# Performance work log

Hardware: AMD Instinct MI355X
Metric: run time of the kernel (lower is better)

Reference implementation:

```python
import jax, jax.numpy as jnp
import numpy as np

D_MODEL = 2048
N_HEADS = 16
D_K = D_MODEL // N_HEADS


def setup_inputs() -> dict:
    key = jax.random.key(0)
    ks = jax.random.split(key, 9)
    s = 1.0 / np.sqrt(D_MODEL)
    def lin(k):
        kw, kb = jax.random.split(k)
        W = jax.random.uniform(kw, (D_MODEL, D_MODEL), jnp.float32, -s, s)
        b = jax.random.uniform(kb, (D_MODEL,), jnp.float32, -s, s)
        return W, b
    Wq, bq = lin(ks[0])
    Wk, bk = lin(ks[1])
    Wv, bv = lin(ks[2])
    Wo, bo = lin(ks[3])
    x = jax.random.normal(ks[4], (2, 2048, D_MODEL), jnp.float32)
    return {"x": x, "Wq": Wq, "bq": bq, "Wk": Wk, "bk": bk,
            "Wv": Wv, "bv": bv, "Wo": Wo, "bo": bo}


def _mha(x, Wq, bq, Wk, bk, Wv, bv, Wo, bo):
    B, S, _ = x.shape
    # Linear projections (torch Linear: x @ W.T + b), split into heads: b s (h d) -> b h s d
    def proj(W, b):
        y = jnp.einsum('bsm,nm->bsn', x, W) + b
        return y.reshape(B, S, N_HEADS, D_K).transpose(0, 2, 1, 3)
    q = proj(Wq, bq)
    k = proj(Wk, bk)
    v = proj(Wv, bv)
    scores = jnp.einsum('bhsd,bhtd->bhst', q, k) / jnp.sqrt(jnp.float32(D_K))
    causal = jnp.triu(jnp.ones((S, S), bool), k=1)  # True above diagonal -> masked
    scores = jnp.where(causal[None, None], -jnp.inf, scores)
    attn = jax.nn.softmax(scores, axis=-1)  # dropout p=0 (eval)
    out = jnp.einsum('bhst,bhtd->bhsd', attn, v)
    out = out.transpose(0, 2, 1, 3).reshape(B, S, D_MODEL)
    return jnp.einsum('bsm,nm->bsn', out, Wo) + bo


def reference(x, Wq, bq, Wk, bk, Wv, bv, Wo, bo):
    return _mha(x, Wq, bq, Wk, bk, Wv, bv, Wo, bo)
```

## Files before the change

kernel.cpp:

```cpp
#include <hip/hip_runtime.h>

typedef unsigned short u16;
typedef __attribute__((ext_vector_type(8))) short bf16x8;
typedef __attribute__((ext_vector_type(4))) float f32x4;
typedef __attribute__((ext_vector_type(4))) unsigned short u16x4;

__device__ __forceinline__ u16 f2bf(float f) {
  union { float f; unsigned u; } v; v.f = f;
  return (u16)((v.u + 0x7FFFu + ((v.u >> 16) & 1u)) >> 16);
}

__device__ __forceinline__ void gload16(const u16* g, u16* l) {
  __builtin_amdgcn_global_load_lds((const __attribute__((address_space(1))) void*)g,
                                   (__attribute__((address_space(3))) void*)l, 16, 0, 0);
}

__global__ __launch_bounds__(256) void k_f2bf5(
    const float* __restrict__ i0, const float* __restrict__ i1, const float* __restrict__ i2,
    const float* __restrict__ i3, const float* __restrict__ i4,
    u16* o0, u16* o1, u16* o2, u16* o3, u16* o4, int n4x, int n4w) {
  const int seg = blockIdx.y;
  const float* in = (seg == 0) ? i0 : (seg == 1) ? i1 : (seg == 2) ? i2 : (seg == 3) ? i3 : i4;
  u16* out = (seg == 0) ? o0 : (seg == 1) ? o1 : (seg == 2) ? o2 : (seg == 3) ? o3 : o4;
  const int n4 = (seg == 0) ? n4x : n4w;
  int i = blockIdx.x * 256 + threadIdx.x;
  const int stride = gridDim.x * 256;
  for (; i < n4; i += stride) {
    const float4 v = ((const float4*)in)[i];
    u16x4 o;
    o.x = f2bf(v.x); o.y = f2bf(v.y); o.z = f2bf(v.z); o.w = f2bf(v.w);
    ((u16x4*)out)[i] = o;
  }
}

template <int OUT_F32>
__global__ __launch_bounds__(256, 4) void k_gemm12(
    const u16* __restrict__ A, const u16* __restrict__ Bt,
    const float* __restrict__ b0, const float* __restrict__ b1, const float* __restrict__ b2,
    u16* __restrict__ C0, u16* __restrict__ C1, u16* __restrict__ C2,
    float* __restrict__ Cf, int NBM)
{
  __shared__ alignas(16) u16 As[8192];
  __shared__ alignas(16) u16 Bs[8192];

  const int tid = threadIdx.x;
  const int lane = tid & 63, wid = tid >> 6;
  const int fr = lane & 15, fg = lane >> 4;
  const int wr = wid >> 1, wc = wid & 1;

  const int nblk = gridDim.x;
  const int q = nblk >> 3, r = nblk & 7;
  const int xcd = blockIdx.x & 7, lid = blockIdx.x >> 3;
  const int wgid = (xcd < r ? xcd * (q + 1) : r * (q + 1) + (xcd - r) * q) + lid;
  const int mb = wgid % NBM, nb = wgid / NBM;
  const long row0 = (long)mb * 128;
  const long col0 = (long)nb * 128;

  int sRow[4], sCol[4];
#pragma unroll
  for (int i = 0; i < 4; ++i) {
    const int g = (wid * 4 + i) * 64 + lane;
    sRow[i] = g >> 3;
    sCol[i] = ((g & 7) ^ (sRow[i] & 7)) << 3;
  }

  const int sw = fr & 7;
  const int aBase = (wr * 64 + fr) * 64;
  const int bBase = (wc * 64 + fr) * 64;
  const int pc0 = (fg ^ sw) << 3;
  const int pc1 = ((4 + fg) ^ sw) << 3;

  f32x4 acc[4][4] = {};

#pragma unroll 1
  for (int t = 0; t < 32; ++t) {
    if (t) __syncthreads();
    const long k0 = (long)t << 6;
#pragma unroll
    for (int i = 0; i < 4; ++i) {
      gload16(A  + (row0 + sRow[i]) * 2048L + k0 + sCol[i], &As[(wid * 4 + i) * 512]);
      gload16(Bt + (col0 + sRow[i]) * 2048L + k0 + sCol[i], &Bs[(wid * 4 + i) * 512]);
    }
    __syncthreads();

#pragma unroll
    for (int kc = 0; kc < 2; ++kc) {
      const int pc = kc ? pc1 : pc0;
      bf16x8 a[4], b[4];
#pragma unroll
      for (int i = 0; i < 4; ++i) {
        a[i] = *(const bf16x8*)&As[aBase + i * 1024 + pc];
        b[i] = *(const bf16x8*)&Bs[bBase + i * 1024 + pc];
      }
#pragma unroll
      for (int i = 0; i < 4; ++i)
#pragma unroll
        for (int j = 0; j < 4; ++j)
          acc[i][j] = __builtin_amdgcn_mfma_f32_16x16x32_bf16(a[i], b[j], acc[i][j], 0, 0, 0);
    }
  }

  const int seg = (int)(col0 >> 11);
  const long colL = col0 & 2047;
  const float* bp = (seg == 0) ? b0 : (seg == 1) ? b1 : b2;
  u16* Cb = (seg == 0) ? C0 : (seg == 1) ? C1 : C2;
#pragma unroll
  for (int j = 0; j < 4; ++j) {
    const long cN = colL + wc * 64 + j * 16 + fr;
    const float bv = bp[cN];
#pragma unroll
    for (int i = 0; i < 4; ++i) {
      const long rM = row0 + wr * 64 + i * 16 + fg * 4;
#pragma unroll
      for (int reg = 0; reg < 4; ++reg) {
        const float v = acc[i][j][reg] + bv;
        if (OUT_F32) Cf[(rM + reg) * 2048 + cN] = v;
        else         Cb[(rM + reg) * 2048 + cN] = f2bf(v);
      }
    }
  }
}

__global__ __launch_bounds__(256) void k_transpose_v(const u16* __restrict__ V,
                                                     u16* __restrict__ Vt) {
  __shared__ u16 t[64][68];
  const int bh = blockIdx.z;
  const long s0 = (long)blockIdx.x * 64;
  const long d0 = (long)blockIdx.y * 64;
  const int tid = threadIdx.x;
  const long rowbase = (long)(bh >> 4) * 2048;
  const int hcol = (bh & 15) * 128;
#pragma unroll
  for (int i = 0; i < 4; ++i) {
    const int v = tid + i * 256;
    const int r = v >> 4, c4 = (v & 15) << 2;
    const u16x4 val = *(const u16x4*)&V[(rowbase + s0 + r) * 2048 + hcol + d0 + c4];
    *(u16x4*)&t[r][c4] = val;
  }
  __syncthreads();
#pragma unroll
  for (int i = 0; i < 4; ++i) {
    const int v = tid + i * 256;
    const int dr = v >> 4, s4 = (v & 15) << 2;
    u16x4 o;
    o.x = t[s4 + 0][dr]; o.y = t[s4 + 1][dr]; o.z = t[s4 + 2][dr]; o.w = t[s4 + 3][dr];
    *(u16x4*)&Vt[((long)bh * 128 + d0 + dr) * 2048 + s0 + s4] = o;
  }
}

__global__ __launch_bounds__(512) void k_flash_attn(
    const u16* __restrict__ Q, const u16* __restrict__ K, const u16* __restrict__ Vt,
    u16* __restrict__ O)
{
  __shared__ alignas(16) u16 Kt[2][8192];
  __shared__ alignas(16) u16 Vtt[2][8192];
  __shared__ alignas(16) u16 Plds[8][16][72];

  const int tid = threadIdx.x;
  const int lane = tid & 63, wid = tid >> 6;
  const int fr = lane & 15, fg = lane >> 4;

  const int L = blockIdx.x;
  const int bh = (L & 7) * 4 + ((L >> 3) & 3);
  const int bx = L >> 5;

  const long rowbase = (long)(bh >> 4) * 2048;
  const int hcol = (bh & 15) * 128;
  const u16* Kg = K + rowbase * 2048 + hcol;
  const u16* Vg = Vt + (long)bh * 128 * 2048;
  const float scale2 = 0.08838834764831845f * 1.44269504089f;

  int kR[2], kC[2], vR[2], vC[2];
#pragma unroll
  for (int i = 0; i < 2; ++i) {
    const int chunk = (wid * 2 + i) * 64 + lane;
    kR[i] = chunk >> 4;
    kC[i] = ((chunk & 15) ^ (kR[i] & 7)) << 3;
    vR[i] = chunk >> 3;
    vC[i] = ((chunk & 7) ^ (vR[i] & 7)) << 3;
  }

  const int sw = fr & 7;
  int kbase[4], vbase[2];
#pragma unroll
  for (int c = 0; c < 4; ++c) kbase[c] = fr * 128 + (((c * 4 + fg) ^ sw) << 3);
#pragma unroll
  for (int kc = 0; kc < 2; ++kc) vbase[kc] = fr * 64 + (((kc * 4 + fg) ^ sw) << 3);

  for (int pass = 0; pass < 2; ++pass) {
    const int qblk = pass ? (15 - bx) : bx;
    const int n = 2 * (qblk + 1);
    const int q_lo = qblk * 128 + wid * 16;

    bf16x8 qf[4];
#pragma unroll
    for (int c = 0; c < 4; ++c)
      qf[c] = *(const bf16x8*)&Q[(rowbase + q_lo + fr) * 2048 + hcol + c * 32 + fg * 8];

    f32x4 oacc[8] = {};
    float m_run[4], l_run[4];
#pragma unroll
    for (int r = 0; r < 4; ++r) { m_run[r] = -1e30f; l_run[r] = 0.0f; }

#pragma unroll
    for (int i = 0; i < 2; ++i) {
      gload16(Kg + (long)kR[i] * 2048 + kC[i], &Kt[0][(wid * 2 + i) * 512]);
      gload16(Vg + (long)vR[i] * 2048 + vC[i], &Vtt[0][(wid * 2 + i) * 512]);
    }

    int cur = 0;
    for (int j = 0; j < n; ++j) {
      if (j + 1 < n) {
        const long kv = (long)(j + 1) * 64;
#pragma unroll
        for (int i = 0; i < 2; ++i) {
          gload16(Kg + (kv + kR[i]) * 2048 + kC[i], &Kt[cur ^ 1][(wid * 2 + i) * 512]);
          gload16(Vg + (long)vR[i] * 2048 + kv + vC[i], &Vtt[cur ^ 1][(wid * 2 + i) * 512]);
        }
        asm volatile("s_waitcnt vmcnt(4)" ::: "memory");
      } else {
        asm volatile("s_waitcnt vmcnt(0)" ::: "memory");
      }
      __builtin_amdgcn_s_barrier();
      __builtin_amdgcn_sched_barrier(0);

      const int kvlo = j * 64;
      const bool skip = (kvlo >= q_lo + 16);
      if (!skip) {
        const bool needmask = (kvlo + 63 > q_lo);

        f32x4 st[4] = {};
        const u16* kt = Kt[cur];
#pragma unroll
        for (int t = 0; t < 4; ++t)
#pragma unroll
          for (int c = 0; c < 4; ++c) {
            const bf16x8 kf = *(const bf16x8*)&kt[kbase[c] + t * 2048];
            st[t] = __builtin_amdgcn_mfma_f32_16x16x32_bf16(qf[c], kf, st[t], 0, 0, 0);
          }

        float pmax[4] = {-1e30f, -1e30f, -1e30f, -1e30f};
        if (needmask) {
#pragma unroll
          for (int t = 0; t < 4; ++t) {
            const int kg = kvlo + t * 16 + fr;
#pragma unroll
            for (int r = 0; r < 4; ++r) {
              const int qg = q_lo + fg * 4 + r;
              const float v = (kg <= qg) ? st[t][r] * scale2 : -1e30f;
              st[t][r] = v;
              pmax[r] = fmaxf(pmax[r], v);
            }
          }
        } else {
#pragma unroll
          for (int t = 0; t < 4; ++t)
#pragma unroll
            for (int r = 0; r < 4; ++r) {
              const float v = st[t][r] * scale2;
              st[t][r] = v;
              pmax[r] = fmaxf(pmax[r], v);
            }
        }
#pragma unroll
        for (int d = 1; d < 16; d <<= 1)
#pragma unroll
          for (int r = 0; r < 4; ++r) pmax[r] = fmaxf(pmax[r], __shfl_xor(pmax[r], d));

        const int ok = (pmax[0] <= m_run[0] + 8.f) & (pmax[1] <= m_run[1] + 8.f) &
                       (pmax[2] <= m_run[2] + 8.f) & (pmax[3] <= m_run[3] + 8.f);
        if (!__all(ok)) {
#pragma unroll
          for (int r = 0; r < 4; ++r) {
            const float nm = fmaxf(m_run[r], pmax[r]);
            const float al = exp2f(m_run[r] - nm);
            l_run[r] *= al;
            m_run[r] = nm;
#pragma unroll
            for (int dt = 0; dt < 8; ++dt) oacc[dt][r] *= al;
          }
        }

        float lsum[4] = {0.f, 0.f, 0.f, 0.f};
#pragma unroll
        for (int t = 0; t < 4; ++t)
#pragma unroll
          for (int r = 0; r < 4; ++r) {
            const float p = exp2f(st[t][r] - m_run[r]);
            st[t][r] = p;
            lsum[r] += p;
          }
#pragma unroll
        for (int d = 1; d < 16; d <<= 1)
#pragma unroll
          for (int r = 0; r < 4; ++r) lsum[r] += __shfl_xor(lsum[r], d);
#pragma unroll
        for (int r = 0; r < 4; ++r) l_run[r] += lsum[r];

#pragma unroll
        for (int t = 0; t < 4; ++t)
#pragma unroll
          for (int r = 0; r < 4; ++r)
            Plds[wid][fg * 4 + r][t * 16 + fr] = f2bf(st[t][r]);
        asm volatile("s_waitcnt lgkmcnt(0)" ::: "memory");
        __builtin_amdgcn_sched_barrier(0);

        const u16* vt = Vtt[cur];
#pragma unroll
        for (int kc = 0; kc < 2; ++kc) {
          const bf16x8 pf = *(const bf16x8*)&Plds[wid][fr][kc * 32 + fg * 8];
#pragma unroll
          for (int dt = 0; dt < 8; ++dt) {
            const bf16x8 vf = *(const bf16x8*)&vt[vbase[kc] + dt * 1024];
            oacc[dt] = __builtin_amdgcn_mfma_f32_16x16x32_bf16(pf, vf, oacc[dt], 0, 0, 0);
          }
        }
      }

      asm volatile("" ::: "memory");
      __builtin_amdgcn_s_barrier();
      cur ^= 1;
    }

    float inv[4];
#pragma unroll
    for (int r = 0; r < 4; ++r) inv[r] = 1.0f / l_run[r];
#pragma unroll
    for (int dt = 0; dt < 8; ++dt)
#pragma unroll
      for (int r = 0; r < 4; ++r)
        O[(rowbase + q_lo + fg * 4 + r) * 2048 + hcol + dt * 16 + fr] = f2bf(oacc[dt][r] * inv[r]);
  }
}

extern "C" void kernel_launch(void* const* d_in, const int* in_sizes, int n_in,
                              void* d_out, int out_size, void* d_ws, size_t ws_size,
                              hipStream_t stream) {
  const float* x  = (const float*)d_in[0];
  const float* Wq = (const float*)d_in[1];
  const float* bq = (const float*)d_in[2];
  const float* Wk = (const float*)d_in[3];
  const float* bk = (const float*)d_in[4];
  const float* Wv = (const float*)d_in[5];
  const float* bv = (const float*)d_in[6];
  const float* Wo = (const float*)d_in[7];
  const float* bo = (const float*)d_in[8];
  float* out = (float*)d_out;

  char* ws = (char*)d_ws;
  const size_t SZ_X = 16777216;
  const size_t SZ_W = 8388608;
  u16* xb  = (u16*)(ws);
  u16* wqb = (u16*)(ws + SZ_X);
  u16* wkb = (u16*)(ws + SZ_X + 1 * SZ_W);
  u16* wvb = (u16*)(ws + SZ_X + 2 * SZ_W);
  u16* wob = (u16*)(ws + SZ_X + 3 * SZ_W);
  u16* Qb  = (u16*)(ws + 1 * SZ_X + 4 * SZ_W);
  u16* Kb  = (u16*)(ws + 2 * SZ_X + 4 * SZ_W);
  u16* Vb  = (u16*)(ws + 3 * SZ_X + 4 * SZ_W);
  u16* Vtb = (u16*)(ws + 4 * SZ_X + 4 * SZ_W);
  u16* Ob  = Vb;

  k_f2bf5<<<dim3(1024, 5), 256, 0, stream>>>(x, Wq, Wk, Wv, Wo,
                                             xb, wqb, wkb, wvb, wob,
                                             8388608 / 4, 4194304 / 4);

  k_gemm12<0><<<1536, 256, 0, stream>>>(xb, wqb, bq, bk, bv, Qb, Kb, Vb, nullptr, 32);

  k_transpose_v<<<dim3(32, 2, 32), 256, 0, stream>>>(Vb, Vtb);

  k_flash_attn<<<256, 512, 0, stream>>>(Qb, Kb, Vtb, Ob);

  k_gemm12<1><<<512, 256, 0, stream>>>(Ob, wob, bo, bo, bo, nullptr, nullptr, nullptr, out, 32);
}
```

Before: 280.1 us.

## Fuse V transpose into QKV GEMM epilogue and retile flash attention

```diff
diff --git a/kernel.cpp b/kernel.cpp
--- a/kernel.cpp
+++ b/kernel.cpp
@@ -37,7 +37,7 @@
 __global__ __launch_bounds__(256, 4) void k_gemm12(
     const u16* __restrict__ A, const u16* __restrict__ Bt,
     const float* __restrict__ b0, const float* __restrict__ b1, const float* __restrict__ b2,
-    u16* __restrict__ C0, u16* __restrict__ C1, u16* __restrict__ C2,
+    u16* __restrict__ C0, u16* __restrict__ C1, u16* __restrict__ Vt,
     float* __restrict__ Cf, int NBM)
 {
   __shared__ alignas(16) u16 As[8192];
@@ -103,7 +103,6 @@
   const int seg = (int)(col0 >> 11);
   const long colL = col0 & 2047;
   const float* bp = (seg == 0) ? b0 : (seg == 1) ? b1 : b2;
-  u16* Cb = (seg == 0) ? C0 : (seg == 1) ? C1 : C2;
 #pragma unroll
   for (int j = 0; j < 4; ++j) {
     const long cN = colL + wc * 64 + j * 16 + fr;
@@ -111,50 +110,34 @@
 #pragma unroll
     for (int i = 0; i < 4; ++i) {
       const long rM = row0 + wr * 64 + i * 16 + fg * 4;
-#pragma unroll
-      for (int reg = 0; reg < 4; ++reg) {
-        const float v = acc[i][j][reg] + bv;
-        if (OUT_F32) Cf[(rM + reg) * 2048 + cN] = v;
-        else         Cb[(rM + reg) * 2048 + cN] = f2bf(v);
+      if (OUT_F32) {
+#pragma unroll
+        for (int reg = 0; reg < 4; ++reg)
+          Cf[(rM + reg) * 2048 + cN] = acc[i][j][reg] + bv;
+      } else if (seg == 2) {
+        const long b = rM >> 11, s0 = rM & 2047;
+        const long h = cN >> 7, d = cN & 127;
+        u16x4 o;
+#pragma unroll
+        for (int reg = 0; reg < 4; ++reg) o[reg] = f2bf(acc[i][j][reg] + bv);
+        *(u16x4*)&Vt[((b * 16 + h) * 128 + d) * 2048 + s0] = o;
+      } else {
+        u16* Cb = (seg == 0) ? C0 : C1;
+#pragma unroll
+        for (int reg = 0; reg < 4; ++reg)
+          Cb[(rM + reg) * 2048 + cN] = f2bf(acc[i][j][reg] + bv);
       }
     }
   }
 }
 
-__global__ __launch_bounds__(256) void k_transpose_v(const u16* __restrict__ V,
-                                                     u16* __restrict__ Vt) {
-  __shared__ u16 t[64][68];
-  const int bh = blockIdx.z;
-  const long s0 = (long)blockIdx.x * 64;
-  const long d0 = (long)blockIdx.y * 64;
-  const int tid = threadIdx.x;
-  const long rowbase = (long)(bh >> 4) * 2048;
-  const int hcol = (bh & 15) * 128;
-#pragma unroll
-  for (int i = 0; i < 4; ++i) {
-    const int v = tid + i * 256;
-    const int r = v >> 4, c4 = (v & 15) << 2;
-    const u16x4 val = *(const u16x4*)&V[(rowbase + s0 + r) * 2048 + hcol + d0 + c4];
-    *(u16x4*)&t[r][c4] = val;
-  }
-  __syncthreads();
-#pragma unroll
-  for (int i = 0; i < 4; ++i) {
-    const int v = tid + i * 256;
-    const int dr = v >> 4, s4 = (v & 15) << 2;
-    u16x4 o;
-    o.x = t[s4 + 0][dr]; o.y = t[s4 + 1][dr]; o.z = t[s4 + 2][dr]; o.w = t[s4 + 3][dr];
-    *(u16x4*)&Vt[((long)bh * 128 + d0 + dr) * 2048 + s0 + s4] = o;
-  }
-}
-
-__global__ __launch_bounds__(512) void k_flash_attn(
+__global__ __launch_bounds__(256, 3) void k_flash_attn(
     const u16* __restrict__ Q, const u16* __restrict__ K, const u16* __restrict__ Vt,
     u16* __restrict__ O)
 {
-  __shared__ alignas(16) u16 Kt[2][8192];
-  __shared__ alignas(16) u16 Vtt[2][8192];
-  __shared__ alignas(16) u16 Plds[8][16][72];
+  __shared__ alignas(16) u16 Kt[8192];
+  __shared__ alignas(16) u16 Vtt[8192];
+  __shared__ alignas(16) u16 Plds[4][16][72];
 
   const int tid = threadIdx.x;
   const int lane = tid & 63, wid = tid >> 6;
@@ -170,14 +153,14 @@
   const u16* Vg = Vt + (long)bh * 128 * 2048;
   const float scale2 = 0.08838834764831845f * 1.44269504089f;
 
-  int kR[2], kC[2], vR[2], vC[2];
-#pragma unroll
-  for (int i = 0; i < 2; ++i) {
-    const int chunk = (wid * 2 + i) * 64 + lane;
-    kR[i] = chunk >> 4;
-    kC[i] = ((chunk & 15) ^ (kR[i] & 7)) << 3;
-    vR[i] = chunk >> 3;
-    vC[i] = ((chunk & 7) ^ (vR[i] & 7)) << 3;
+  int kR[4], kC[4], vR[4], vC[4];
+#pragma unroll
+  for (int i = 0; i < 4; ++i) {
+    const int g = (wid * 4 + i) * 64 + lane;
+    kR[i] = g >> 4;
+    kC[i] = ((g & 15) ^ (kR[i] & 7)) << 3;
+    vR[i] = g >> 3;
+    vC[i] = ((g & 7) ^ (vR[i] & 7)) << 3;
   }
 
   const int sw = fr & 7;
@@ -188,9 +171,9 @@
   for (int kc = 0; kc < 2; ++kc) vbase[kc] = fr * 64 + (((kc * 4 + fg) ^ sw) << 3);
 
   for (int pass = 0; pass < 2; ++pass) {
-    const int qblk = pass ? (15 - bx) : bx;
-    const int n = 2 * (qblk + 1);
-    const int q_lo = qblk * 128 + wid * 16;
+    const int qblk = pass ? (31 - bx) : bx;
+    const int n = qblk + 1;
+    const int q_lo = qblk * 64 + wid * 16;
 
     bf16x8 qf[4];
 #pragma unroll
@@ -202,27 +185,15 @@
 #pragma unroll
     for (int r = 0; r < 4; ++r) { m_run[r] = -1e30f; l_run[r] = 0.0f; }
 
-#pragma unroll
-    for (int i = 0; i < 2; ++i) {
-      gload16(Kg + (long)kR[i] * 2048 + kC[i], &Kt[0][(wid * 2 + i) * 512]);
-      gload16(Vg + (long)vR[i] * 2048 + vC[i], &Vtt[0][(wid * 2 + i) * 512]);
-    }
-
-    int cur = 0;
     for (int j = 0; j < n; ++j) {
-      if (j + 1 < n) {
-        const long kv = (long)(j + 1) * 64;
-#pragma unroll
-        for (int i = 0; i < 2; ++i) {
-          gload16(Kg + (kv + kR[i]) * 2048 + kC[i], &Kt[cur ^ 1][(wid * 2 + i) * 512]);
-          gload16(Vg + (long)vR[i] * 2048 + kv + vC[i], &Vtt[cur ^ 1][(wid * 2 + i) * 512]);
-        }
-        asm volatile("s_waitcnt vmcnt(4)" ::: "memory");
-      } else {
-        asm volatile("s_waitcnt vmcnt(0)" ::: "memory");
+      if (j | pass) __syncthreads();
+      const long kv = (long)j * 64;
+#pragma unroll
+      for (int i = 0; i < 4; ++i) {
+        gload16(Kg + (kv + kR[i]) * 2048 + kC[i], &Kt[(wid * 4 + i) * 512]);
+        gload16(Vg + (long)vR[i] * 2048 + kv + vC[i], &Vtt[(wid * 4 + i) * 512]);
       }
-      __builtin_amdgcn_s_barrier();
-      __builtin_amdgcn_sched_barrier(0);
+      __syncthreads();
 
       const int kvlo = j * 64;
       const bool skip = (kvlo >= q_lo + 16);
@@ -230,12 +201,11 @@
         const bool needmask = (kvlo + 63 > q_lo);
 
         f32x4 st[4] = {};
-        const u16* kt = Kt[cur];
 #pragma unroll
         for (int t = 0; t < 4; ++t)
 #pragma unroll
           for (int c = 0; c < 4; ++c) {
-            const bf16x8 kf = *(const bf16x8*)&kt[kbase[c] + t * 2048];
+            const bf16x8 kf = *(const bf16x8*)&Kt[kbase[c] + t * 2048];
             st[t] = __builtin_amdgcn_mfma_f32_16x16x32_bf16(qf[c], kf, st[t], 0, 0, 0);
           }
 
@@ -305,21 +275,16 @@
         asm volatile("s_waitcnt lgkmcnt(0)" ::: "memory");
         __builtin_amdgcn_sched_barrier(0);
 
-        const u16* vt = Vtt[cur];
 #pragma unroll
         for (int kc = 0; kc < 2; ++kc) {
           const bf16x8 pf = *(const bf16x8*)&Plds[wid][fr][kc * 32 + fg * 8];
 #pragma unroll
           for (int dt = 0; dt < 8; ++dt) {
-            const bf16x8 vf = *(const bf16x8*)&vt[vbase[kc] + dt * 1024];
+            const bf16x8 vf = *(const bf16x8*)&Vtt[vbase[kc] + dt * 1024];
             oacc[dt] = __builtin_amdgcn_mfma_f32_16x16x32_bf16(pf, vf, oacc[dt], 0, 0, 0);
           }
         }
       }
-
-      asm volatile("" ::: "memory");
-      __builtin_amdgcn_s_barrier();
-      cur ^= 1;
     }
 
     float inv[4];
@@ -365,11 +330,9 @@
                                              xb, wqb, wkb, wvb, wob,
                                              8388608 / 4, 4194304 / 4);
 
-  k_gemm12<0><<<1536, 256, 0, stream>>>(xb, wqb, bq, bk, bv, Qb, Kb, Vb, nullptr, 32);
-
-  k_transpose_v<<<dim3(32, 2, 32), 256, 0, stream>>>(Vb, Vtb);
-
-  k_flash_attn<<<256, 512, 0, stream>>>(Qb, Kb, Vtb, Ob);
+  k_gemm12<0><<<1536, 256, 0, stream>>>(xb, wqb, bq, bk, bv, Qb, Kb, Vtb, nullptr, 32);
+
+  k_flash_attn<<<512, 256, 0, stream>>>(Qb, Kb, Vtb, Ob);
 
   k_gemm12<1><<<512, 256, 0, stream>>>(Ob, wob, bo, bo, bo, nullptr, nullptr, nullptr, out, 32);
 }
```

Result: no change. 281.0 us (+0.3%).
